# Kernel tuning notes

Hardware: AMD Instinct MI355X
Metric: run time of the kernel (lower is better)

Reference implementation:

```python
import jax, jax.numpy as jnp
import numpy as np

B, S, H = 2, 2048, 2048
NQ, NKV = 32, 8          # query heads, kv heads
G = NQ // NKV            # query groups per kv head
D = H // NQ              # head dim = 64
MAX_POS = 4096
THETA = 10000.0


def _rope_tables(position_ids):
    # freqs per the original apply_rotary_emb (interleaved pair convention)
    freqs = 1.0 / THETA ** (jnp.arange(0, D, 2)[: D // 2].astype(jnp.float32) / D)
    t = jnp.arange(MAX_POS, dtype=jnp.float32)
    ang = jnp.outer(t, freqs)                     # [MAX_POS, D/2]
    cos = jnp.take(jnp.cos(ang), position_ids, axis=0)[:, :, None, :]  # [B,S,1,D/2]
    sin = jnp.take(jnp.sin(ang), position_ids, axis=0)[:, :, None, :]
    return cos, sin


def _apply_rope(x, cos, sin):
    # x: [B,S,h,D]; pairs are interleaved (x0,x1),(x2,x3),...
    x2 = x.astype(jnp.float32).reshape(*x.shape[:-1], D // 2, 2)
    xr, xi = x2[..., 0], x2[..., 1]
    out_r = xr * cos - xi * sin
    out_i = xr * sin + xi * cos
    return jnp.stack((out_r, out_i), axis=-1).reshape(x.shape).astype(x.dtype)


def setup_inputs() -> dict:
    key = jax.random.key(0)
    ks = jax.random.split(key, 5)
    init_scale = 0.02 / np.sqrt(H)
    hidden_states = jax.random.normal(ks[0], (B, S, H), dtype=jnp.float32)
    wq = jax.random.normal(ks[1], (H, H), dtype=jnp.float32) * init_scale
    wk = jax.random.normal(ks[2], (H, H // G), dtype=jnp.float32) * init_scale
    wv = jax.random.normal(ks[3], (H, H // G), dtype=jnp.float32) * init_scale
    wo = jax.random.normal(ks[4], (H, H), dtype=jnp.float32) * init_scale
    attention_mask = jnp.ones((B, S), dtype=jnp.int32)
    position_ids = jnp.broadcast_to(jnp.arange(S, dtype=jnp.int32), (B, S))
    return dict(hidden_states=hidden_states, attention_mask=attention_mask,
                position_ids=position_ids, wq=wq, wk=wk, wv=wv, wo=wo)


def reference(hidden_states, attention_mask, position_ids, wq, wk, wv, wo):
    # projections (no bias)
    xq = (hidden_states @ wq).reshape(B, S, NQ, D)
    xk = (hidden_states @ wk).reshape(B, S, NKV, D)
    xv = (hidden_states @ wv).reshape(B, S, NKV, D)
    # GQA repeat: kv head h -> query heads h*G .. h*G+G-1 (consecutive)
    xk = jnp.repeat(xk, G, axis=2)  # [B,S,NQ,D]
    xv = jnp.repeat(xv, G, axis=2)

    cos, sin = _rope_tables(position_ids)
    xq = _apply_rope(xq, cos, sin)
    xk = _apply_rope(xk, cos, sin)

    # causal + padding mask -> additive bias
    causal = jnp.tril(jnp.ones((S, S), dtype=bool))[None, None]          # [1,1,S,S]
    pad = (attention_mask > 0)[:, None, None, :]                          # [B,1,1,S]
    combined = jnp.logical_and(causal, pad)                               # [B,1,S,S]
    neg = jnp.finfo(jnp.float32).min
    bias = jnp.where(combined, 0.0, neg).astype(jnp.float32)

    scale = 1.0 / np.sqrt(D)
    scores = jnp.einsum('bqhd,bkhd->bhqk', xq, xk).astype(jnp.float32) * scale
    scores = scores + bias
    attn = jax.nn.softmax(scores, axis=-1)                                # [B,NQ,S,S] fp32
    out = jnp.einsum('bhqk,bkhd->bqhd', attn, xv)                         # [B,S,NQ,D]
    out = out.reshape(B, S, H)
    return out @ wo
```

## Files before the change

kernel.cpp:

```cpp
#include <hip/hip_runtime.h>
#include <cstdint>

typedef __attribute__((ext_vector_type(8))) __bf16  bf8v;
typedef __attribute__((ext_vector_type(4))) float   f4v;
typedef __attribute__((ext_vector_type(4))) short   s4v;
typedef __attribute__((ext_vector_type(8))) unsigned short ush8;

__device__ __forceinline__ float bf2f(unsigned short u) {
    union { unsigned u; float f; } v; v.u = ((unsigned)u) << 16; return v.f;
}
__device__ __forceinline__ unsigned short f2bf(float f) {
    union { float f; unsigned u; } v; v.f = f;
    unsigned u = v.u;
    return (unsigned short)((u + 0x7fffu + ((u >> 16) & 1u)) >> 16);
}
__device__ __forceinline__ unsigned short f2bf_n(float f) {
    union { __bf16 h; unsigned short s; } v; v.h = (__bf16)f; return v.s;
}
__device__ __forceinline__ unsigned pack2bf(float a, float b) {
    union { __bf16 h[2]; unsigned u; } v;
    v.h[0] = (__bf16)a; v.h[1] = (__bf16)b; return v.u;
}

#define GLDS16(gp, lp)                                                          \
    __builtin_amdgcn_global_load_lds(                                           \
        (const __attribute__((address_space(1))) void*)(uintptr_t)(gp),         \
        (__attribute__((address_space(3))) void*)(uintptr_t)(lp), 16, 0, 0)

__global__ void cast_f32_to_bf16(const float* __restrict__ in,
                                 unsigned short* __restrict__ out, int n8) {
    int i = blockIdx.x * 256 + threadIdx.x;
    if (i >= n8) return;
    float4 a = ((const float4*)in)[2 * i];
    float4 b = ((const float4*)in)[2 * i + 1];
    ush8 o;
    o[0] = f2bf(a.x); o[1] = f2bf(a.y); o[2] = f2bf(a.z); o[3] = f2bf(a.w);
    o[4] = f2bf(b.x); o[5] = f2bf(b.y); o[6] = f2bf(b.z); o[7] = f2bf(b.w);
    ((ush8*)out)[i] = o;
}

__global__ void transpose_cast(const float* __restrict__ in,
                               unsigned short* __restrict__ out, int R, int C) {
    __shared__ float t[32][33];
    int c0 = blockIdx.x * 32, r0 = blockIdx.y * 32;
    int x = threadIdx.x, y = threadIdx.y;
    #pragma unroll
    for (int i = 0; i < 32; i += 8) t[y + i][x] = in[(size_t)(r0 + y + i) * C + c0 + x];
    __syncthreads();
    #pragma unroll
    for (int i = 0; i < 32; i += 8)
        out[(size_t)(c0 + y + i) * R + r0 + x] = f2bf(t[x][y + i]);
}

__global__ void transpose_v_bf16(const unsigned short* __restrict__ in,
                                 unsigned short* __restrict__ out) {
    __shared__ unsigned short t[32][33];
    int c0 = blockIdx.x * 32;
    int r0 = blockIdx.y * 32;
    int x = threadIdx.x, y = threadIdx.y;
    #pragma unroll
    for (int i = 0; i < 32; i += 8)
        t[y + i][x] = in[(size_t)(r0 + y + i) * 3072 + 2560 + c0 + x];
    __syncthreads();
    #pragma unroll
    for (int i = 0; i < 32; i += 8)
        out[(size_t)(c0 + y + i) * 4096 + r0 + x] = t[x][y + i];
}

__global__ void rope_strided(unsigned short* __restrict__ X,
                             const int* __restrict__ pos_ids,
                             int coloff, int stride, int nh_log2) {
    int idx = blockIdx.x * 256 + threadIdx.x;
    int i   = idx & 31;
    int hh  = (idx >> 5) & ((1 << nh_log2) - 1);
    int tok = idx >> (5 + nh_log2);
    int pos = pos_ids[tok];
    float ang = (float)pos * exp2f(-0.41524101186092f * (float)i);
    float s = sinf(ang), c = cosf(ang);
    unsigned short* p = X + (size_t)tok * stride + coloff + hh * 64 + 2 * i;
    unsigned pr = *(const unsigned*)p;
    float xr = bf2f((unsigned short)(pr & 0xffff));
    float xi = bf2f((unsigned short)(pr >> 16));
    float orr = xr * c - xi * s;
    float oi  = xr * s + xi * c;
    *(unsigned*)p = (unsigned)f2bf(orr) | ((unsigned)f2bf(oi) << 16);
}

template <int OUT_BF16>
__global__ __launch_bounds__(256) void gemm_bt(const unsigned short* __restrict__ A,
                                               const unsigned short* __restrict__ Bt,
                                               void* __restrict__ Cv, int N, int K) {
    __shared__ __align__(16) unsigned short As[128 * 64];
    __shared__ __align__(16) unsigned short Bs[128 * 64];
    const int t = threadIdx.x;
    const int lane = t & 63, w = t >> 6;
    const int wr = w >> 1, wc = w & 1;
    const int lr = lane & 15, lh = lane >> 4;
    const int m0 = blockIdx.y * 128, n0 = blockIdx.x * 128;

    f4v acc[4][4];
    #pragma unroll
    for (int i = 0; i < 4; ++i)
        #pragma unroll
        for (int j = 0; j < 4; ++j) acc[i][j] = f4v{0.f, 0.f, 0.f, 0.f};

    const int o_t = t * 16;
    for (int k0 = 0; k0 < K; k0 += 64) {
        __syncthreads();
        #pragma unroll
        for (int s = 0; s < 4; ++s) {
            int o = s * 4096 + o_t;
            int row = o >> 7;
            int src = (o & 127) ^ ((row & 7) << 4);
            const unsigned short* gA = A + (size_t)(m0 + row) * K + k0 + (src >> 1);
            GLDS16(gA, As + (o >> 1));
            const unsigned short* gB = Bt + (size_t)(n0 + row) * K + k0 + (src >> 1);
            GLDS16(gB, Bs + (o >> 1));
        }
        __syncthreads();
        #pragma unroll
        for (int kk = 0; kk < 2; ++kk) {
            bf8v af[4], bfr[4];
            #pragma unroll
            for (int mi = 0; mi < 4; ++mi) {
                int row = wr * 64 + mi * 16 + lr;
                int col = (kk * 32 + lh * 8) ^ ((row & 7) << 3);
                af[mi] = *(const bf8v*)(As + row * 64 + col);
            }
            #pragma unroll
            for (int ni = 0; ni < 4; ++ni) {
                int row = wc * 64 + ni * 16 + lr;
                int col = (kk * 32 + lh * 8) ^ ((row & 7) << 3);
                bfr[ni] = *(const bf8v*)(Bs + row * 64 + col);
            }
            #pragma unroll
            for (int mi = 0; mi < 4; ++mi)
                #pragma unroll
                for (int ni = 0; ni < 4; ++ni)
                    acc[mi][ni] = __builtin_amdgcn_mfma_f32_16x16x32_bf16(
                        af[mi], bfr[ni], acc[mi][ni], 0, 0, 0);
        }
    }
    #pragma unroll
    for (int mi = 0; mi < 4; ++mi)
        #pragma unroll
        for (int ni = 0; ni < 4; ++ni)
            #pragma unroll
            for (int r = 0; r < 4; ++r) {
                int row = m0 + wr * 64 + mi * 16 + lh * 4 + r;
                int col = n0 + wc * 64 + ni * 16 + lr;
                float v = acc[mi][ni][r];
                if (OUT_BF16) ((unsigned short*)Cv)[(size_t)row * N + col] = f2bf(v);
                else          ((float*)Cv)[(size_t)row * N + col] = v;
            }
}

__global__ __launch_bounds__(256, 4) void flash_attn(
        const unsigned short* __restrict__ QKV,
        const unsigned short* __restrict__ VtG,
        const int* __restrict__ amask,
        const int* __restrict__ pos_ids,
        unsigned short* __restrict__ O) {
    __shared__ __align__(16) unsigned short Ks[2][64 * 64];
    __shared__ __align__(16) unsigned short Vs[2][64 * 64];

    const int t = threadIdx.x, lane = t & 63, w = t >> 6;
    const int lr = lane & 15, lh = lane >> 4;
    const int pair = blockIdx.x, h = blockIdx.y, b = blockIdx.z;
    const size_t tok0 = (size_t)b * 2048;

    const unsigned short* Kb = QKV + tok0 * 3072 + 2048 + (h >> 2) * 64;
    const unsigned short* Vb = VtG + (size_t)((h >> 2) * 64) * 4096 + tok0;
    const int* amrow = amask + b * 2048;

#define STAGE(buf, kt)                                                              \
    {   _Pragma("unroll")                                                           \
        for (int s_ = 0; s_ < 2; ++s_) {                                            \
            int c_ = s_ * 256 + t;                                                  \
            int row_ = c_ >> 3;                                                     \
            int sc_ = (((c_ & 7) * 16) ^ ((row_ & 7) << 4)) >> 1;                   \
            GLDS16(Kb + (size_t)((kt) * 64 + row_) * 3072 + sc_, Ks[buf] + c_ * 8); \
            GLDS16(Vb + (size_t)row_ * 4096 + (kt) * 64 + sc_, Vs[buf] + c_ * 8);   \
        }                                                                           \
    }

    const float SCL = 0.18033688011112042f;

    unsigned aliveMaskV = 0;
    {
        const int4* am4 = (const int4*)amrow;
        #pragma unroll
        for (int s = 0; s < 8; ++s) {
            int4 a = am4[s * 64 + lane];
            unsigned long long bal = __ballot(a.x && a.y && a.z && a.w);
            #pragma unroll
            for (int g = 0; g < 4; ++g)
                aliveMaskV |= (((bal >> (16 * g)) & 0xFFFFull) == 0xFFFFull)
                                  ? (1u << (4 * s + g)) : 0u;
        }
    }
    const int aliveMask = __builtin_amdgcn_readfirstlane((int)aliveMaskV);

    int vcol[4];
    #pragma unroll
    for (int kf = 0; kf < 4; ++kf) vcol[kf] = (kf * 16 + lh * 4) ^ ((lr & 7) << 3);

    int cur = 0;

    #pragma unroll 1
    for (int half = 0; half < 2; ++half) {
        const int qt = half ? (31 - pair) : pair;
        const int q0 = qt * 64;
        const int nkv = qt + 1;
        const int qloc = w * 16 + lr;

        const unsigned short* Qp = QKV + (tok0 + q0 + qloc) * 3072 + h * 64;
        union Q8 { bf8v v; unsigned short s[8]; } qa0u, qa1u;
        qa0u.v = *(const bf8v*)(Qp + lh * 8);
        qa1u.v = *(const bf8v*)(Qp + 32 + lh * 8);
        {
            int pos = pos_ids[tok0 + q0 + qloc];
            #pragma unroll
            for (int r = 0; r < 4; ++r) {
                float i0 = (float)(lh * 4 + r);
                float ang0 = (float)pos * exp2f(-0.41524101186092f * i0);
                float sn = sinf(ang0), cs = cosf(ang0);
                float xr = bf2f(qa0u.s[2 * r]), xi = bf2f(qa0u.s[2 * r + 1]);
                qa0u.s[2 * r]     = f2bf_n((xr * cs - xi * sn) * SCL);
                qa0u.s[2 * r + 1] = f2bf_n((xr * sn + xi * cs) * SCL);
                float i1 = (float)(16 + lh * 4 + r);
                float ang1 = (float)pos * exp2f(-0.41524101186092f * i1);
                float sn1 = sinf(ang1), cs1 = cosf(ang1);
                float yr = bf2f(qa1u.s[2 * r]), yi = bf2f(qa1u.s[2 * r + 1]);
                qa1u.s[2 * r]     = f2bf_n((yr * cs1 - yi * sn1) * SCL);
                qa1u.s[2 * r + 1] = f2bf_n((yr * sn1 + yi * cs1) * SCL);
            }
        }
        const bf8v qa0 = qa0u.v, qa1 = qa1u.v;

        f4v oacc[4];
        #pragma unroll
        for (int i = 0; i < 4; ++i) oacc[i] = f4v{0.f, 0.f, 0.f, 0.f};
        float m_ = -1e30f, l_ = 0.f;

        STAGE(cur, 0);
        __syncthreads();

        #pragma unroll 1
        for (int kt = 0; kt < nkv; ++kt) {
            if (kt + 1 < nkv) STAGE(cur ^ 1, kt + 1);

            f4v sa[4];
            #pragma unroll
            for (int kf = 0; kf < 4; ++kf) sa[kf] = f4v{0.f, 0.f, 0.f, 0.f};
            __builtin_amdgcn_s_setprio(1);
            #pragma unroll
            for (int kk = 0; kk < 2; ++kk) {
                bf8v qa = kk ? qa1 : qa0;
                int col = kk * 32 + lh * 8;
                #pragma unroll
                for (int kf = 0; kf < 4; ++kf) {
                    bf8v kb = *(const bf8v*)(Ks[cur] + (kf * 16 + lr) * 64 + (col ^ ((lr & 7) << 3)));
                    sa[kf] = __builtin_amdgcn_mfma_f32_16x16x32_bf16(kb, qa, sa[kf], 0, 0, 0);
                }
            }
            __builtin_amdgcn_s_setprio(0);

            const bool diag = (kt == qt);
            const bool tileAlive = ((aliveMask >> kt) & 1) != 0;

            float pvv[4][4];
            if (tileAlive && !diag) {
                #pragma unroll
                for (int kf = 0; kf < 4; ++kf)
                    #pragma unroll
                    for (int r = 0; r < 4; ++r) pvv[kf][r] = sa[kf][r];
            } else if (tileAlive) {
                #pragma unroll
                for (int kf = 0; kf < 4; ++kf)
                    #pragma unroll
                    for (int r = 0; r < 4; ++r) {
                        int keyl = kf * 16 + lh * 4 + r;
                        pvv[kf][r] = (keyl > qloc) ? -1e30f : sa[kf][r];
                    }
            } else {
                int amv[4][4];
                #pragma unroll
                for (int kf = 0; kf < 4; ++kf) {
                    int4 aq = *(const int4*)(amrow + kt * 64 + kf * 16 + lh * 4);
                    amv[kf][0] = aq.x; amv[kf][1] = aq.y; amv[kf][2] = aq.z; amv[kf][3] = aq.w;
                }
                #pragma unroll
                for (int kf = 0; kf < 4; ++kf)
                    #pragma unroll
                    for (int r = 0; r < 4; ++r) {
                        int keyl = kf * 16 + lh * 4 + r;
                        bool dead = (amv[kf][r] == 0) || (diag && keyl > qloc);
                        pvv[kf][r] = dead ? -1e30f : sa[kf][r];
                    }
            }

            float t0 = fmaxf(fmaxf(pvv[0][0], pvv[0][1]), fmaxf(pvv[0][2], pvv[0][3]));
            float t1 = fmaxf(fmaxf(pvv[1][0], pvv[1][1]), fmaxf(pvv[1][2], pvv[1][3]));
            float t2 = fmaxf(fmaxf(pvv[2][0], pvv[2][1]), fmaxf(pvv[2][2], pvv[2][3]));
            float t3 = fmaxf(fmaxf(pvv[3][0], pvv[3][1]), fmaxf(pvv[3][2], pvv[3][3]));
            float mx = fmaxf(fmaxf(t0, t1), fmaxf(t2, t3));
            mx = fmaxf(mx, __shfl_xor(mx, 16));
            mx = fmaxf(mx, __shfl_xor(mx, 32));

            if (!__all(mx <= m_ + 8.0f)) {
                float mn = fmaxf(m_, mx);
                float fac = exp2f(m_ - mn);
                m_ = mn;
                l_ *= fac;
                float facr[4];
                #pragma unroll
                for (int r = 0; r < 4; ++r) facr[r] = __shfl(fac, lh * 4 + r);
                #pragma unroll
                for (int df = 0; df < 4; ++df) {
                    f4v o = oacc[df];
                    o[0] *= facr[0]; o[1] *= facr[1]; o[2] *= facr[2]; o[3] *= facr[3];
                    oacc[df] = o;
                }
            }

            float pe[4][4];
            #pragma unroll
            for (int kf = 0; kf < 4; ++kf)
                #pragma unroll
                for (int r = 0; r < 4; ++r)
                    pe[kf][r] = exp2f(pvv[kf][r] - m_);
            float s0 = (pe[0][0] + pe[0][1]) + (pe[0][2] + pe[0][3]);
            float s1 = (pe[1][0] + pe[1][1]) + (pe[1][2] + pe[1][3]);
            float s2 = (pe[2][0] + pe[2][1]) + (pe[2][2] + pe[2][3]);
            float s3 = (pe[3][0] + pe[3][1]) + (pe[3][2] + pe[3][3]);
            float rs = (s0 + s1) + (s2 + s3);
            rs += __shfl_xor(rs, 16);
            rs += __shfl_xor(rs, 32);
            l_ += rs;

            __builtin_amdgcn_s_setprio(1);
            #pragma unroll
            for (int kf = 0; kf < 4; ++kf) {
                union { uint2 u; s4v s; } pa;
                pa.u.x = pack2bf(pe[kf][0], pe[kf][1]);
                pa.u.y = pack2bf(pe[kf][2], pe[kf][3]);
                #pragma unroll
                for (int df = 0; df < 4; ++df) {
                    const s4v vb = *(const s4v*)(Vs[cur] + (df * 16 + lr) * 64 + vcol[kf]);
                    oacc[df] = __builtin_amdgcn_mfma_f32_16x16x16bf16_1k(
                        pa.s, vb, oacc[df], 0, 0, 0);
                }
            }
            __builtin_amdgcn_s_setprio(0);

            __syncthreads();
            cur ^= 1;
        }

        float invl = 1.0f / l_;
        float invr[4];
        #pragma unroll
        for (int r = 0; r < 4; ++r) invr[r] = __shfl(invl, lh * 4 + r);
        #pragma unroll
        for (int df = 0; df < 4; ++df)
            #pragma unroll
            for (int r = 0; r < 4; ++r) {
                int qg = q0 + w * 16 + lh * 4 + r;
                float v = oacc[df][r] * invr[r];
                O[(tok0 + qg) * 2048 + h * 64 + df * 16 + lr] = f2bf_n(v);
            }
    }
#undef STAGE
}

extern "C" void kernel_launch(void* const* d_in, const int* in_sizes, int n_in,
                              void* d_out, int out_size, void* d_ws, size_t ws_size,
                              hipStream_t stream) {
    const float* hs   = (const float*)d_in[0];
    const int* amask  = (const int*)d_in[1];
    const int* pos    = (const int*)d_in[2];
    const float* wq   = (const float*)d_in[3];
    const float* wk   = (const float*)d_in[4];
    const float* wv   = (const float*)d_in[5];
    const float* wo   = (const float*)d_in[6];

    char* ws = (char*)d_ws;
    unsigned short* Xb   = (unsigned short*)(ws);
    unsigned short* Wqkv = (unsigned short*)(ws + 16777216);
    unsigned short* Wot  = (unsigned short*)(ws + 29360128);
    unsigned short* AOb  = (unsigned short*)(ws + 37748736);

    char* ob = (char*)d_out;
    unsigned short* QKV = (unsigned short*)ob;
    unsigned short* VtG = (unsigned short*)(ob + 25165824);

    cast_f32_to_bf16<<<4096, 256, 0, stream>>>(hs, Xb, 1048576);
    transpose_cast<<<dim3(64, 64), dim3(32, 8), 0, stream>>>(wq, Wqkv, 2048, 2048);
    transpose_cast<<<dim3(16, 64), dim3(32, 8), 0, stream>>>(wk, Wqkv + 4194304, 2048, 512);
    transpose_cast<<<dim3(16, 64), dim3(32, 8), 0, stream>>>(wv, Wqkv + 5242880, 2048, 512);
    transpose_cast<<<dim3(64, 64), dim3(32, 8), 0, stream>>>(wo, Wot, 2048, 2048);

    gemm_bt<1><<<dim3(24, 32), 256, 0, stream>>>(Xb, Wqkv, (void*)QKV, 3072, 2048);

    rope_strided<<<4096, 256, 0, stream>>>(QKV, pos, 2048, 3072, 3);

    transpose_v_bf16<<<dim3(16, 128), dim3(32, 8), 0, stream>>>(QKV, VtG);

    flash_attn<<<dim3(16, 32, 2), 256, 0, stream>>>(QKV, VtG, amask, pos, AOb);

    gemm_bt<0><<<dim3(16, 32), 256, 0, stream>>>(AOb, Wot, d_out, 2048, 2048);
}
```

Baseline: 224.6 us.

## Pre-swizzle transposed V in global memory and use hardware bf16 conversion

The V transpose kernel now writes tokens in a per-row XOR-swizzled order (groups of 4 tokens permuted by the low bits of d). The attention kernel's V staging therefore copies contiguous 16-byte chunks, and its LDS read offsets are changed to match the new swizzle, which is meant to cut LDS bank conflicts on V fragment reads. Separately, the manual round-to-nearest-even float-to-bf16 routine is replaced by the compiler's native bf16 conversion and packed conversions in the cast, rope and GEMM epilogue paths. The V layout change couples the producer and consumer kernels, so any index mismatch would corrupt results.

```diff
diff --git a/kernel.cpp b/kernel.cpp
--- a/kernel.cpp
+++ b/kernel.cpp
@@ -8,11 +8,6 @@
 
 __device__ __forceinline__ float bf2f(unsigned short u) {
     union { unsigned u; float f; } v; v.u = ((unsigned)u) << 16; return v.f;
-}
-__device__ __forceinline__ unsigned short f2bf(float f) {
-    union { float f; unsigned u; } v; v.f = f;
-    unsigned u = v.u;
-    return (unsigned short)((u + 0x7fffu + ((u >> 16) & 1u)) >> 16);
 }
 __device__ __forceinline__ unsigned short f2bf_n(float f) {
     union { __bf16 h; unsigned short s; } v; v.h = (__bf16)f; return v.s;
@@ -33,10 +28,12 @@
     if (i >= n8) return;
     float4 a = ((const float4*)in)[2 * i];
     float4 b = ((const float4*)in)[2 * i + 1];
-    ush8 o;
-    o[0] = f2bf(a.x); o[1] = f2bf(a.y); o[2] = f2bf(a.z); o[3] = f2bf(a.w);
-    o[4] = f2bf(b.x); o[5] = f2bf(b.y); o[6] = f2bf(b.z); o[7] = f2bf(b.w);
-    ((ush8*)out)[i] = o;
+    uint4 o;
+    o.x = pack2bf(a.x, a.y);
+    o.y = pack2bf(a.z, a.w);
+    o.z = pack2bf(b.x, b.y);
+    o.w = pack2bf(b.z, b.w);
+    ((uint4*)out)[i] = o;
 }
 
 __global__ void transpose_cast(const float* __restrict__ in,
@@ -49,7 +46,7 @@
     __syncthreads();
     #pragma unroll
     for (int i = 0; i < 32; i += 8)
-        out[(size_t)(c0 + y + i) * R + r0 + x] = f2bf(t[x][y + i]);
+        out[(size_t)(c0 + y + i) * R + r0 + x] = f2bf_n(t[x][y + i]);
 }
 
 __global__ void transpose_v_bf16(const unsigned short* __restrict__ in,
@@ -63,8 +60,13 @@
         t[y + i][x] = in[(size_t)(r0 + y + i) * 3072 + 2560 + c0 + x];
     __syncthreads();
     #pragma unroll
-    for (int i = 0; i < 32; i += 8)
-        out[(size_t)(c0 + y + i) * 4096 + r0 + x] = t[x][y + i];
+    for (int i = 0; i < 32; i += 8) {
+        int d   = c0 + y + i;
+        int tok = r0 + x;
+        int g   = (tok >> 2) & 15;
+        int tp  = (tok & ~63) | (((g ^ (d & 15)) << 2)) | (tok & 3);
+        out[(size_t)d * 4096 + tp] = t[x][y + i];
+    }
 }
 
 __global__ void rope_strided(unsigned short* __restrict__ X,
@@ -83,7 +85,7 @@
     float xi = bf2f((unsigned short)(pr >> 16));
     float orr = xr * c - xi * s;
     float oi  = xr * s + xi * c;
-    *(unsigned*)p = (unsigned)f2bf(orr) | ((unsigned)f2bf(oi) << 16);
+    *(unsigned*)p = pack2bf(orr, oi);
 }
 
 template <int OUT_BF16>
@@ -150,7 +152,7 @@
                 int row = m0 + wr * 64 + mi * 16 + lh * 4 + r;
                 int col = n0 + wc * 64 + ni * 16 + lr;
                 float v = acc[mi][ni][r];
-                if (OUT_BF16) ((unsigned short*)Cv)[(size_t)row * N + col] = f2bf(v);
+                if (OUT_BF16) ((unsigned short*)Cv)[(size_t)row * N + col] = f2bf_n(v);
                 else          ((float*)Cv)[(size_t)row * N + col] = v;
             }
 }
@@ -180,7 +182,8 @@
             int row_ = c_ >> 3;                                                     \
             int sc_ = (((c_ & 7) * 16) ^ ((row_ & 7) << 4)) >> 1;                   \
             GLDS16(Kb + (size_t)((kt) * 64 + row_) * 3072 + sc_, Ks[buf] + c_ * 8); \
-            GLDS16(Vb + (size_t)row_ * 4096 + (kt) * 64 + sc_, Vs[buf] + c_ * 8);   \
+            GLDS16(Vb + (size_t)row_ * 4096 + (kt) * 64 + (c_ & 7) * 8,             \
+                   Vs[buf] + c_ * 8);                                               \
         }                                                                           \
     }
 
@@ -203,7 +206,7 @@
 
     int vcol[4];
     #pragma unroll
-    for (int kf = 0; kf < 4; ++kf) vcol[kf] = (kf * 16 + lh * 4) ^ ((lr & 7) << 3);
+    for (int kf = 0; kf < 4; ++kf) vcol[kf] = ((kf * 4 + lh) ^ lr) * 4;
 
     int cur = 0;
 
```

Result: no change. 223.5 us (-0.5%).
